# Kernel optimization log

Measured on AMD Instinct MI355X. Metric: run time of the kernel, lower is better.

The kernel has to match this reference:

```python
import jax, jax.numpy as jnp
import numpy as np

LN_EPS = 1e-5


def setup_inputs() -> dict:
    key = jax.random.key(0)
    k_x, k_w = jax.random.split(key)
    B, T, F, M = 128, 512, 512, 512
    x = jax.random.normal(k_x, (B, T, F), dtype=jnp.float32)
    gamma = jnp.ones((T,), dtype=jnp.float32)
    beta = jnp.zeros((T,), dtype=jnp.float32)
    W = jax.random.normal(k_w, (M, T), dtype=jnp.float32) * 0.02  # Linear(T -> M) weight
    b = jnp.zeros((M,), dtype=jnp.float32)
    return {"x": x, "gamma": gamma, "beta": beta, "W": W, "b": b}


def reference(x, gamma, beta, W, b):
    # x: [B, T, F]. LayerNorm over the time axis T per (batch, feature) row,
    # matching norm(x.permute(0,2,1).reshape(-1, T)).
    mean = jnp.mean(x, axis=1, keepdims=True)                 # [B,1,F]
    var = jnp.mean((x - mean) ** 2, axis=1, keepdims=True)     # [B,1,F]
    xn = (x - mean) * jax.lax.rsqrt(var + LN_EPS)
    xn = xn * gamma[None, :, None] + beta[None, :, None]       # [B,T,F]
    # time_mlp: Linear along T (applied to [B,F,T] rows), output [B,F,M]
    # expressed directly in [B,T,F] layout -> [B,M,F]
    y = jnp.einsum('btf,mt->bmf', xn, W) + b[None, :, None]
    y = jax.nn.gelu(y, approximate=False)                      # torch nn.GELU is exact
    # dropout_prob = 0.0 -> identity; residual (M == T)
    return y + x
```

## Files before the change

### kernel.cpp

```cpp
#include <hip/hip_runtime.h>
#include <hip/hip_bf16.h>
#include <cstdint>


#define B_ 128
#define T_ 512
#define F_ 512
#define M_ 512
#define FT 32
#define XN_STRIDE 520

typedef __attribute__((ext_vector_type(8))) short bf16x8;
typedef __attribute__((ext_vector_type(4))) float f32x4;

static __device__ __forceinline__ unsigned short f2bf(float f) {
    unsigned int u = __float_as_uint(f);
    unsigned int r = u + 0x7FFFu + ((u >> 16) & 1u);
    return (unsigned short)(r >> 16);
}

static __device__ __forceinline__ float gelu_fast(float y) {
    float y2 = y * y;
    float u  = y * (-1.5957691216057308f - 0.07135481283262997f * y2);
    float s  = __expf(u);
    return y * __builtin_amdgcn_rcpf(1.0f + s);
}

__global__ void wconv_kernel(const float* __restrict__ W, unsigned short* __restrict__ Wq) {
    int idx  = blockIdx.x * 256 + threadIdx.x;
    int lane = idx & 63;
    int mg   = (idx >> 6) & 31;
    int kc   = idx >> 11;
    int m = mg * 16 + (lane & 15);
    int k = kc * 32 + (lane >> 4) * 8;
    const float* src = W + (size_t)m * 512 + k;
    float4 v0 = *(const float4*)(src);
    float4 v1 = *(const float4*)(src + 4);
    uint4 o;
    o.x = (unsigned int)f2bf(v0.x) | ((unsigned int)f2bf(v0.y) << 16);
    o.y = (unsigned int)f2bf(v0.z) | ((unsigned int)f2bf(v0.w) << 16);
    o.z = (unsigned int)f2bf(v1.x) | ((unsigned int)f2bf(v1.y) << 16);
    o.w = (unsigned int)f2bf(v1.z) | ((unsigned int)f2bf(v1.w) << 16);
    *(uint4*)(Wq + (size_t)idx * 8) = o;
}

__global__ __launch_bounds__(512, 4) void timemix_main(
    const float* __restrict__ x, const float* __restrict__ gamma,
    const float* __restrict__ beta, const unsigned short* __restrict__ Wq,
    const float* __restrict__ bias, float* __restrict__ out)
{
    __shared__ __align__(16) unsigned char smem[37632];
    unsigned char* xnS = smem;
    float* gS    = (float*)(smem + 33280);
    float* bS    = (float*)(smem + 35328);
    float* meanS = (float*)(smem + 37376);
    float* rstdS = (float*)(smem + 37504);
    float* red_sum = (float*)(smem);
    float* red_sq  = (float*)(smem + 2048);

    const int tid   = threadIdx.x;
    const int w     = tid >> 6;
    const int lane  = tid & 63;
    const int batch = blockIdx.y;
    const int f0    = blockIdx.x * FT;

    gS[tid] = gamma[tid];
    bS[tid] = beta[tid];

    const int f  = lane & 31;
    const int tg = w * 2 + (lane >> 5);
    float xv[32];
    {
        const float* xb = x + ((size_t)batch * T_ + (size_t)tg * 32) * F_ + f0 + f;
        float s = 0.f, q = 0.f;
        #pragma unroll
        for (int i = 0; i < 32; ++i) {
            float v = xb[(size_t)i * F_];
            xv[i] = v; s += v; q += v * v;
        }
        red_sum[tg * 32 + f] = s;
        red_sq [tg * 32 + f] = q;
    }
    __syncthreads();

    if (tid < 32) {
        float s = 0.f, q = 0.f;
        #pragma unroll
        for (int g = 0; g < 16; ++g) { s += red_sum[g * 32 + tid]; q += red_sq[g * 32 + tid]; }
        float mean = s * (1.0f / 512.0f);
        float var  = q * (1.0f / 512.0f) - mean * mean;
        meanS[tid] = mean;
        rstdS[tid] = rsqrtf(var + 1e-5f);
    }
    __syncthreads();

    {
        const float mean = meanS[f];
        const float rstd = rstdS[f];
        #pragma unroll
        for (int c = 0; c < 4; ++c) {
            const int t0 = tg * 32 + c * 8;
            unsigned int pr[4];
            #pragma unroll
            for (int h = 0; h < 4; ++h) {
                float a0 = rstd * gS[t0 + 2 * h];
                float v0 = xv[c * 8 + 2 * h] * a0 + (bS[t0 + 2 * h] - mean * a0);
                float a1 = rstd * gS[t0 + 2 * h + 1];
                float v1 = xv[c * 8 + 2 * h + 1] * a1 + (bS[t0 + 2 * h + 1] - mean * a1);
                pr[h] = (unsigned int)f2bf(v0) | ((unsigned int)f2bf(v1) << 16);
            }
            uint4 pk; pk.x = pr[0]; pk.y = pr[1]; pk.z = pr[2]; pk.w = pr[3];
            *(uint4*)(xnS + (size_t)f * (XN_STRIDE * 2) + t0 * 2) = pk;
        }
    }
    __syncthreads();

    const int lr = lane & 15;
    const int q4 = lane >> 4;
    const unsigned short* wbase = Wq + ((size_t)(w * 4) * 64 + lane) * 8;

    f32x4 acc[4][2];
    #pragma unroll
    for (int mi = 0; mi < 4; ++mi)
        #pragma unroll
        for (int fi = 0; fi < 2; ++fi)
            acc[mi][fi] = (f32x4){0.f, 0.f, 0.f, 0.f};

    bf16x8 aA[4], aB[4];
    #pragma unroll
    for (int mi = 0; mi < 4; ++mi)
        aA[mi] = *(const bf16x8*)(wbase + (size_t)mi * 512);

    for (int kc = 0; kc < 16; kc += 2) {
        #pragma unroll
        for (int mi = 0; mi < 4; ++mi)
            aB[mi] = *(const bf16x8*)(wbase + (size_t)(kc + 1) * 16384 + (size_t)mi * 512);
        {
            bf16x8 b0 = *(const bf16x8*)(xnS + (size_t)lr * (XN_STRIDE * 2) + kc * 64 + q4 * 16);
            bf16x8 b1 = *(const bf16x8*)(xnS + (size_t)(16 + lr) * (XN_STRIDE * 2) + kc * 64 + q4 * 16);
            #pragma unroll
            for (int mi = 0; mi < 4; ++mi) {
                acc[mi][0] = __builtin_amdgcn_mfma_f32_16x16x32_bf16(aA[mi], b0, acc[mi][0], 0, 0, 0);
                acc[mi][1] = __builtin_amdgcn_mfma_f32_16x16x32_bf16(aA[mi], b1, acc[mi][1], 0, 0, 0);
            }
        }
        if (kc + 2 < 16) {
            #pragma unroll
            for (int mi = 0; mi < 4; ++mi)
                aA[mi] = *(const bf16x8*)(wbase + (size_t)(kc + 2) * 16384 + (size_t)mi * 512);
        }
        {
            bf16x8 b0 = *(const bf16x8*)(xnS + (size_t)lr * (XN_STRIDE * 2) + (kc + 1) * 64 + q4 * 16);
            bf16x8 b1 = *(const bf16x8*)(xnS + (size_t)(16 + lr) * (XN_STRIDE * 2) + (kc + 1) * 64 + q4 * 16);
            #pragma unroll
            for (int mi = 0; mi < 4; ++mi) {
                acc[mi][0] = __builtin_amdgcn_mfma_f32_16x16x32_bf16(aB[mi], b0, acc[mi][0], 0, 0, 0);
                acc[mi][1] = __builtin_amdgcn_mfma_f32_16x16x32_bf16(aB[mi], b1, acc[mi][1], 0, 0, 0);
            }
        }
    }

    #pragma unroll
    for (int mi = 0; mi < 4; ++mi) {
        const int mbase = w * 64 + mi * 16 + q4 * 4;
        #pragma unroll
        for (int r = 0; r < 4; ++r) {
            const int m = mbase + r;
            const float bv = bias[m];
            #pragma unroll
            for (int fi = 0; fi < 2; ++fi) {
                float y = acc[mi][fi][r] + bv;
                float gl = gelu_fast(y);
                size_t o = ((size_t)(batch * 512 + m)) * 512 + (size_t)(f0 + fi * 16 + lr);
                out[o] = gl + x[o];
            }
        }
    }
}

extern "C" void kernel_launch(void* const* d_in, const int* in_sizes, int n_in,
                              void* d_out, int out_size, void* d_ws, size_t ws_size,
                              hipStream_t stream) {
    const float* x     = (const float*)d_in[0];
    const float* gamma = (const float*)d_in[1];
    const float* beta  = (const float*)d_in[2];
    const float* W     = (const float*)d_in[3];
    const float* bias  = (const float*)d_in[4];
    float* out = (float*)d_out;
    unsigned short* Wq = (unsigned short*)d_ws;

    wconv_kernel<<<dim3(128), 256, 0, stream>>>(W, Wq);
    dim3 grid(F_ / FT, B_);
    timemix_main<<<grid, 512, 0, stream>>>(x, gamma, beta, Wq, bias, out);
}
```

Baseline: 297.0 us.

## Widen feature tile to 64 and re-read x instead of caching in registers

Doubles the per-block feature tile from 32 to 64 columns, so each block computes a 512x64 output tile and halves the number of times the bf16 weight matrix is streamed per batch. Each wave now owns 64 time rows over all 64 features, and x is read twice from global memory (once for statistics, once for normalization) instead of being held in 32 registers. LDS grows to about 71KB per block, which limits occupancy, and the accumulator count doubles, adding register pressure.

```diff
diff --git a/kernel.cpp b/kernel.cpp
--- a/kernel.cpp
+++ b/kernel.cpp
@@ -7,7 +7,7 @@
 #define T_ 512
 #define F_ 512
 #define M_ 512
-#define FT 32
+#define FT 64
 #define XN_STRIDE 520
 
 typedef __attribute__((ext_vector_type(8))) short bf16x8;
@@ -49,12 +49,12 @@
     const float* __restrict__ beta, const unsigned short* __restrict__ Wq,
     const float* __restrict__ bias, float* __restrict__ out)
 {
-    __shared__ __align__(16) unsigned char smem[37632];
+    __shared__ __align__(16) unsigned char smem[71168];
     unsigned char* xnS = smem;
-    float* gS    = (float*)(smem + 33280);
-    float* bS    = (float*)(smem + 35328);
-    float* meanS = (float*)(smem + 37376);
-    float* rstdS = (float*)(smem + 37504);
+    float* gS    = (float*)(smem + 66560);
+    float* bS    = (float*)(smem + 68608);
+    float* meanS = (float*)(smem + 70656);
+    float* rstdS = (float*)(smem + 70912);
     float* red_sum = (float*)(smem);
     float* red_sq  = (float*)(smem + 2048);
 
@@ -67,26 +67,23 @@
     gS[tid] = gamma[tid];
     bS[tid] = beta[tid];
 
-    const int f  = lane & 31;
-    const int tg = w * 2 + (lane >> 5);
-    float xv[32];
+    const float* xb = x + ((size_t)batch * T_ + (size_t)w * 64) * F_ + f0 + lane;
     {
-        const float* xb = x + ((size_t)batch * T_ + (size_t)tg * 32) * F_ + f0 + f;
         float s = 0.f, q = 0.f;
         #pragma unroll
-        for (int i = 0; i < 32; ++i) {
+        for (int i = 0; i < 64; ++i) {
             float v = xb[(size_t)i * F_];
-            xv[i] = v; s += v; q += v * v;
-        }
-        red_sum[tg * 32 + f] = s;
-        red_sq [tg * 32 + f] = q;
+            s += v; q += v * v;
+        }
+        red_sum[w * 64 + lane] = s;
+        red_sq [w * 64 + lane] = q;
     }
     __syncthreads();
 
-    if (tid < 32) {
+    if (tid < 64) {
         float s = 0.f, q = 0.f;
         #pragma unroll
-        for (int g = 0; g < 16; ++g) { s += red_sum[g * 32 + tid]; q += red_sq[g * 32 + tid]; }
+        for (int g = 0; g < 8; ++g) { s += red_sum[g * 64 + tid]; q += red_sq[g * 64 + tid]; }
         float mean = s * (1.0f / 512.0f);
         float var  = q * (1.0f / 512.0f) - mean * mean;
         meanS[tid] = mean;
@@ -95,22 +92,26 @@
     __syncthreads();
 
     {
-        const float mean = meanS[f];
-        const float rstd = rstdS[f];
-        #pragma unroll
-        for (int c = 0; c < 4; ++c) {
-            const int t0 = tg * 32 + c * 8;
+        const float mean = meanS[lane];
+        const float rstd = rstdS[lane];
+        unsigned char* xrow = xnS + (size_t)lane * (XN_STRIDE * 2);
+        #pragma unroll
+        for (int c = 0; c < 8; ++c) {
+            const int t0 = w * 64 + c * 8;
+            float v[8];
+            #pragma unroll
+            for (int i = 0; i < 8; ++i) v[i] = xb[(size_t)(c * 8 + i) * F_];
             unsigned int pr[4];
             #pragma unroll
             for (int h = 0; h < 4; ++h) {
                 float a0 = rstd * gS[t0 + 2 * h];
-                float v0 = xv[c * 8 + 2 * h] * a0 + (bS[t0 + 2 * h] - mean * a0);
+                float v0 = v[2 * h] * a0 + (bS[t0 + 2 * h] - mean * a0);
                 float a1 = rstd * gS[t0 + 2 * h + 1];
-                float v1 = xv[c * 8 + 2 * h + 1] * a1 + (bS[t0 + 2 * h + 1] - mean * a1);
+                float v1 = v[2 * h + 1] * a1 + (bS[t0 + 2 * h + 1] - mean * a1);
                 pr[h] = (unsigned int)f2bf(v0) | ((unsigned int)f2bf(v1) << 16);
             }
             uint4 pk; pk.x = pr[0]; pk.y = pr[1]; pk.z = pr[2]; pk.w = pr[3];
-            *(uint4*)(xnS + (size_t)f * (XN_STRIDE * 2) + t0 * 2) = pk;
+            *(uint4*)(xrow + (size_t)t0 * 2) = pk;
         }
     }
     __syncthreads();
@@ -119,12 +120,14 @@
     const int q4 = lane >> 4;
     const unsigned short* wbase = Wq + ((size_t)(w * 4) * 64 + lane) * 8;
 
-    f32x4 acc[4][2];
+    f32x4 acc[4][4];
     #pragma unroll
     for (int mi = 0; mi < 4; ++mi)
         #pragma unroll
-        for (int fi = 0; fi < 2; ++fi)
+        for (int fi = 0; fi < 4; ++fi)
             acc[mi][fi] = (f32x4){0.f, 0.f, 0.f, 0.f};
+
+    const unsigned char* bbase = xnS + (size_t)lr * (XN_STRIDE * 2) + q4 * 16;
 
     bf16x8 aA[4], aB[4];
     #pragma unroll
@@ -136,13 +139,15 @@
         for (int mi = 0; mi < 4; ++mi)
             aB[mi] = *(const bf16x8*)(wbase + (size_t)(kc + 1) * 16384 + (size_t)mi * 512);
         {
-            bf16x8 b0 = *(const bf16x8*)(xnS + (size_t)lr * (XN_STRIDE * 2) + kc * 64 + q4 * 16);
-            bf16x8 b1 = *(const bf16x8*)(xnS + (size_t)(16 + lr) * (XN_STRIDE * 2) + kc * 64 + q4 * 16);
-            #pragma unroll
-            for (int mi = 0; mi < 4; ++mi) {
-                acc[mi][0] = __builtin_amdgcn_mfma_f32_16x16x32_bf16(aA[mi], b0, acc[mi][0], 0, 0, 0);
-                acc[mi][1] = __builtin_amdgcn_mfma_f32_16x16x32_bf16(aA[mi], b1, acc[mi][1], 0, 0, 0);
-            }
+            bf16x8 b[4];
+            #pragma unroll
+            for (int fi = 0; fi < 4; ++fi)
+                b[fi] = *(const bf16x8*)(bbase + (size_t)fi * 16 * (XN_STRIDE * 2) + kc * 64);
+            #pragma unroll
+            for (int mi = 0; mi < 4; ++mi)
+                #pragma unroll
+                for (int fi = 0; fi < 4; ++fi)
+                    acc[mi][fi] = __builtin_amdgcn_mfma_f32_16x16x32_bf16(aA[mi], b[fi], acc[mi][fi], 0, 0, 0);
         }
         if (kc + 2 < 16) {
             #pragma unroll
@@ -150,13 +155,15 @@
                 aA[mi] = *(const bf16x8*)(wbase + (size_t)(kc + 2) * 16384 + (size_t)mi * 512);
         }
         {
-            bf16x8 b0 = *(const bf16x8*)(xnS + (size_t)lr * (XN_STRIDE * 2) + (kc + 1) * 64 + q4 * 16);
-            bf16x8 b1 = *(const bf16x8*)(xnS + (size_t)(16 + lr) * (XN_STRIDE * 2) + (kc + 1) * 64 + q4 * 16);
-            #pragma unroll
-            for (int mi = 0; mi < 4; ++mi) {
-                acc[mi][0] = __builtin_amdgcn_mfma_f32_16x16x32_bf16(aB[mi], b0, acc[mi][0], 0, 0, 0);
-                acc[mi][1] = __builtin_amdgcn_mfma_f32_16x16x32_bf16(aB[mi], b1, acc[mi][1], 0, 0, 0);
-            }
+            bf16x8 b[4];
+            #pragma unroll
+            for (int fi = 0; fi < 4; ++fi)
+                b[fi] = *(const bf16x8*)(bbase + (size_t)fi * 16 * (XN_STRIDE * 2) + (kc + 1) * 64);
+            #pragma unroll
+            for (int mi = 0; mi < 4; ++mi)
+                #pragma unroll
+                for (int fi = 0; fi < 4; ++fi)
+                    acc[mi][fi] = __builtin_amdgcn_mfma_f32_16x16x32_bf16(aB[mi], b[fi], acc[mi][fi], 0, 0, 0);
         }
     }
 
@@ -168,7 +175,7 @@
             const int m = mbase + r;
             const float bv = bias[m];
             #pragma unroll
-            for (int fi = 0; fi < 2; ++fi) {
+            for (int fi = 0; fi < 4; ++fi) {
                 float y = acc[mi][fi][r] + bv;
                 float gl = gelu_fast(y);
                 size_t o = ((size_t)(batch * 512 + m)) * 512 + (size_t)(f0 + fi * 16 + lr);
```

New measurement: 300.2 us. Within noise of the previous version (+1.1%).
